# Performance work log

Measured on AMD Instinct MI355X. Metric: run time of the kernel, lower is better.

## Reference

```python
import jax, jax.numpy as jnp
import numpy as np
import math

B, T, E, H, HS = 8, 2048, 384, 6, 64

def setup_inputs() -> dict:
    key = jax.random.key(0)
    ks = jax.random.split(key, 5)
    scale = 1.0 / math.sqrt(E)
    return {
        "x": jax.random.normal(ks[0], (B, T, E), dtype=jnp.float32),
        "Wq": jax.random.normal(ks[1], (H, E, HS), dtype=jnp.float32) * scale,
        "Wk": jax.random.normal(ks[2], (H, E, HS), dtype=jnp.float32) * scale,
        "Wv": jax.random.normal(ks[3], (H, E, HS), dtype=jnp.float32) * scale,
        "Wo": jax.random.normal(ks[4], (H, HS, E), dtype=jnp.float32) * (1.0 / math.sqrt(HS)),
    }

def reference(x, Wq, Wk, Wv, Wo):
    # x: [B,T,E]; per-head projections batched over heads.
    q = jnp.einsum('bte,hed->bhtd', x, Wq)  # [B,H,T,HS]
    k = jnp.einsum('bte,hed->bhtd', x, Wk)
    v = jnp.einsum('bte,hed->bhtd', x, Wv)
    scores = jnp.einsum('bhid,bhjd->bhij', q, k)  # [B,H,T,T]
    # Faithful to source: MULTIPLICATIVE tril mask (masked logits become 0, not -inf),
    # then scale by 1/sqrt(head_size), then softmax.
    t = x.shape[1]
    tril = jnp.tril(jnp.ones((t, t), dtype=scores.dtype))
    scores = scores * tril / math.sqrt(HS)
    attn = jax.nn.softmax(scores, axis=-1)
    ctx = jnp.einsum('bhij,bhjd->bhid', attn, v)  # [B,H,T,HS]
    # Per-head output projection to embed dim, summed over heads (source accumulates).
    out = jnp.einsum('bhtd,hde->bte', ctx, Wo)  # [B,T,E]
    return out
```

## Files before the change

### kernel.cpp

```cpp
#include <hip/hip_runtime.h>
#include <math.h>

#define BBATCH 8
#define TSEQ   2048
#define EDIM   384
#define NHEAD  6
#define DHEAD  64
#define NBH    48
#define QTILE  128
#define NQT    16
#define NW1    442368
#define NW2    147456
#define XSZ    6291456
#define KVSZ   6291456

typedef __attribute__((ext_vector_type(8)))  short bf16x8;
typedef __attribute__((ext_vector_type(16))) float f32x16;
typedef __attribute__((ext_vector_type(2)))  int   i32x2;
typedef unsigned short u16;
typedef unsigned int   u32;

#define MFMA(a, b, c) __builtin_amdgcn_mfma_f32_32x32x16_bf16(a, b, c, 0, 0, 0)

__device__ __forceinline__ u16 f2bf(float f) {
  u32 u = __float_as_uint(f);
  return (u16)((u + 0x7fffu + ((u >> 16) & 1u)) >> 16);
}
__device__ __forceinline__ float bf2f(u16 h) {
  return __uint_as_float(((u32)h) << 16);
}
__device__ __forceinline__ bf16x8 mk8(u32 w0, u32 w1, u32 w2, u32 w3) {
  union { u32 u[4]; bf16x8 v; } t;
  t.u[0] = w0; t.u[1] = w1; t.u[2] = w2; t.u[3] = w3;
  return t.v;
}

__global__ __launch_bounds__(256) void prep_w_k(
    const float* __restrict__ Wq, const float* __restrict__ Wk,
    const float* __restrict__ Wv, const float* __restrict__ Wo,
    u16* __restrict__ wtH, u16* __restrict__ wtL,
    u16* __restrict__ woH, u16* __restrict__ woL) {
  int idx = blockIdx.x * 256 + threadIdx.x;
  if (idx < NW1) {
    int d = idx & 63;
    int q = idx >> 6;
    int e = q % EDIM;
    int ph = q / EDIM;
    const float* W = (ph < 6) ? Wq : (ph < 12) ? Wk : Wv;
    int h = ph % 6;
    float v = W[((size_t)h * EDIM + e) * DHEAD + d];
    u16 hi = f2bf(v);
    size_t o = ((size_t)ph * DHEAD + d) * EDIM + e;
    wtH[o] = hi;
    wtL[o] = f2bf(v - bf2f(hi));
  } else {
    int o = idx - NW1;
    int eo = o % EDIM;
    int hd = o / EDIM;
    float v = Wo[(size_t)hd * EDIM + eo];
    u16 hi = f2bf(v);
    size_t oo = (size_t)eo * EDIM + hd;
    woH[oo] = hi;
    woL[oo] = f2bf(v - bf2f(hi));
  }
}

__global__ __launch_bounds__(256) void splitx_k(
    const float* __restrict__ x, u16* __restrict__ xh, u16* __restrict__ xl) {
  int i = (blockIdx.x * 256 + threadIdx.x) * 8;
  float4 a = *(const float4*)(x + i);
  float4 b = *(const float4*)(x + i + 4);
  u16 h0 = f2bf(a.x), h1 = f2bf(a.y), h2 = f2bf(a.z), h3 = f2bf(a.w);
  u16 h4 = f2bf(b.x), h5 = f2bf(b.y), h6 = f2bf(b.z), h7 = f2bf(b.w);
  uint4 H, L;
  H.x = (u32)h0 | ((u32)h1 << 16); H.y = (u32)h2 | ((u32)h3 << 16);
  H.z = (u32)h4 | ((u32)h5 << 16); H.w = (u32)h6 | ((u32)h7 << 16);
  L.x = (u32)f2bf(a.x - bf2f(h0)) | ((u32)f2bf(a.y - bf2f(h1)) << 16);
  L.y = (u32)f2bf(a.z - bf2f(h2)) | ((u32)f2bf(a.w - bf2f(h3)) << 16);
  L.z = (u32)f2bf(b.x - bf2f(h4)) | ((u32)f2bf(b.y - bf2f(h5)) << 16);
  L.w = (u32)f2bf(b.z - bf2f(h6)) | ((u32)f2bf(b.w - bf2f(h7)) << 16);
  *(uint4*)(xh + i) = H;
  *(uint4*)(xl + i) = L;
}

__global__ __launch_bounds__(256, 2) void proj_k(
    const u16* __restrict__ xh, const u16* __restrict__ xl,
    const u16* __restrict__ wtH, const u16* __restrict__ wtL,
    u16* __restrict__ qh, u16* __restrict__ ql,
    u16* __restrict__ kh, u16* __restrict__ kl,
    u16* __restrict__ vTh, u16* __restrict__ vTl,
    float* __restrict__ psum) {
  __shared__ __align__(16) unsigned char sm[32768];
  const int tid = threadIdx.x;
  const int w = tid >> 6, l = tid & 63, lh = l >> 5, l31 = l & 31;
  const int gid = ((blockIdx.x & 7) * 288) + ((int)blockIdx.x >> 3);
  const int bx = gid / 18, ph = gid % 18;
  const int p = ph / 6, h = ph % 6;
  const int bt0 = bx * 128;
  const u16* __restrict__ wBh = wtH + (size_t)ph * DHEAD * EDIM;
  const u16* __restrict__ wBl = wtL + (size_t)ph * DHEAD * EDIM;

  f32x16 acc0, acc1;
#pragma unroll
  for (int i = 0; i < 16; ++i) { acc0[i] = 0.f; acc1[i] = 0.f; }

  for (int k0 = 0; k0 < EDIM; k0 += 64) {
    __syncthreads();
#pragma unroll
    for (int i = 0; i < 4; ++i) {
      int c = tid + i * 256;
      int r = c >> 3, s = c & 7;
      int off = (r * 128 + s * 16) ^ ((r & 7) << 4);
      size_t g = (size_t)(bt0 + r) * EDIM + k0 + s * 8;
      *(uint4*)(sm + off) = *(const uint4*)(xh + g);
      *(uint4*)(sm + 16384 + off) = *(const uint4*)(xl + g);
    }
    __syncthreads();
    const int arow = 32 * w + l31;
#pragma unroll
    for (int ks = 0; ks < 4; ++ks) {
      int aoff = (arow * 128 + ks * 32 + 16 * lh) ^ ((arow & 7) << 4);
      bf16x8 aH = *(const bf16x8*)(sm + aoff);
      bf16x8 aL = *(const bf16x8*)(sm + 16384 + aoff);
      int eoff = k0 + ks * 16 + 8 * lh;
      size_t b0 = (size_t)l31 * EDIM + eoff;
      size_t b1 = (size_t)(32 + l31) * EDIM + eoff;
      bf16x8 bH0 = *(const bf16x8*)(wBh + b0);
      bf16x8 bL0 = *(const bf16x8*)(wBl + b0);
      bf16x8 bH1 = *(const bf16x8*)(wBh + b1);
      bf16x8 bL1 = *(const bf16x8*)(wBl + b1);
      acc0 = MFMA(aH, bH0, acc0); acc0 = MFMA(aH, bL0, acc0); acc0 = MFMA(aL, bH0, acc0);
      acc1 = MFMA(aH, bH1, acc1); acc1 = MFMA(aH, bL1, acc1); acc1 = MFMA(aL, bH1, acc1);
    }
  }

  const int b = bt0 >> 11, t0b = bt0 & (TSEQ - 1);
  const int bh = b * NHEAD + h;
  const float scale = (p == 0) ? 0.125f : 1.0f;

  if (p < 2) {
    u16* oH = (p == 0) ? qh : kh;
    u16* oL = (p == 0) ? ql : kl;
#pragma unroll
    for (int reg = 0; reg < 16; ++reg) {
      int row = (reg & 3) + 8 * (reg >> 2) + 4 * lh + 32 * w;
      size_t base = ((size_t)bh * TSEQ + t0b + row) * DHEAD;
      float v0 = acc0[reg] * scale, v1 = acc1[reg] * scale;
      u16 h0 = f2bf(v0), h1 = f2bf(v1);
      oH[base + l31] = h0;       oL[base + l31] = f2bf(v0 - bf2f(h0));
      oH[base + 32 + l31] = h1;  oL[base + 32 + l31] = f2bf(v1 - bf2f(h1));
    }
  } else {
    u16* T = (u16*)sm;
#pragma unroll
    for (int half = 0; half < 2; ++half) {
      __syncthreads();
#pragma unroll
      for (int reg = 0; reg < 16; ++reg) {
        int t = (reg & 3) + 8 * (reg >> 2) + 4 * lh + 32 * w;
        float v0 = acc0[reg], v1 = acc1[reg];
        u16 e0, e1;
        if (half == 0) { e0 = f2bf(v0); e1 = f2bf(v1); }
        else {
          u16 a0 = f2bf(v0), a1 = f2bf(v1);
          e0 = f2bf(v0 - bf2f(a0)); e1 = f2bf(v1 - bf2f(a1));
        }
        T[l31 * 132 + t] = e0;
        T[(32 + l31) * 132 + t] = e1;
      }
      __syncthreads();
      u16* dst = half ? vTl : vTh;
#pragma unroll
      for (int i = 0; i < 8; ++i) {
        int c = tid + i * 256;
        int d = c >> 5, s = c & 31;
        uint2 val = *(const uint2*)(T + d * 132 + s * 4);
        *(uint2*)(dst + ((size_t)bh * DHEAD + d) * TSEQ + t0b + s * 4) = val;
      }
    }
    float s0 = 0.f, s1 = 0.f;
#pragma unroll
    for (int reg = 0; reg < 16; ++reg) { s0 += acc0[reg]; s1 += acc1[reg]; }
    s0 += __shfl_xor(s0, 32);
    s1 += __shfl_xor(s1, 32);
    __syncthreads();
    float* ps = (float*)sm;
    if (lh == 0) { ps[w * 64 + l31] = s0; ps[w * 64 + 32 + l31] = s1; }
    __syncthreads();
    if (tid < 64) {
      float t = ps[tid] + ps[64 + tid] + ps[128 + tid] + ps[192 + tid];
      int tile = t0b >> 7;
      psum[((size_t)bh * NQT + tile) * DHEAD + tid] = t;
    }
  }
}

__global__ __launch_bounds__(64, 3) void attn_k(
    const u16* __restrict__ qh, const u16* __restrict__ ql,
    const u16* __restrict__ kh, const u16* __restrict__ kl,
    const u16* __restrict__ vTh, const u16* __restrict__ vTl,
    const float* __restrict__ psum,
    u16* __restrict__ cxh, u16* __restrict__ cxl) {
  const int l = threadIdx.x;
  const int lh = l >> 5, l31 = l & 31;
  const int xcd = blockIdx.x & 7;
  const int idx = (int)blockIdx.x >> 3;
  const int qt = (NQT - 1) - (idx / 24);
  const int rem = idx % 24;
  const int bhl = rem >> 2, ws = rem & 3;
  const int bh = xcd * 6 + bhl;
  const int b = bh / NHEAD, h = bh % NHEAD;
  const int t0 = qt * QTILE;
  const size_t kvb = (size_t)bh * TSEQ * DHEAD;

  const int qglo = t0 + 32 * ws;
  bf16x8 qfH[4], qfL[4];
#pragma unroll
  for (int ks = 0; ks < 4; ++ks) {
    size_t g = kvb + (size_t)(qglo + l31) * DHEAD + ks * 16 + 8 * lh;
    qfH[ks] = *(const bf16x8*)(qh + g);
    qfL[ks] = *(const bf16x8*)(ql + g);
  }

  f32x16 accO0, accO1;
#pragma unroll
  for (int i = 0; i < 16; ++i) { accO0[i] = 0.f; accO1[i] = 0.f; }
  float lrun = 0.f;
  const int qg = qglo + l31;
  const int S = 2 * (qt + 1);

  for (int jt = 0; jt < S; ++jt) {
#pragma unroll
    for (int jh = 0; jh < 2; ++jh) {
      f32x16 accSa, accSb;
#pragma unroll
      for (int i = 0; i < 16; ++i) { accSa[i] = 0.f; accSb[i] = 0.f; }
      const size_t krow = kvb + (size_t)(jt * 64 + jh * 32 + l31) * DHEAD;
      __builtin_amdgcn_s_setprio(1);
#pragma unroll
      for (int ks = 0; ks < 4; ++ks) {
        size_t g = krow + ks * 16 + 8 * lh;
        bf16x8 aH = *(const bf16x8*)(kh + g);
        bf16x8 aL = *(const bf16x8*)(kl + g);
        accSa = MFMA(aH, qfH[ks], accSa);
        accSb = MFMA(aH, qfL[ks], accSb);
        accSb = MFMA(aL, qfH[ks], accSb);
      }
      __builtin_amdgcn_s_setprio(0);
      f32x16 accS;
#pragma unroll
      for (int i = 0; i < 16; ++i) accS[i] = accSa[i] + accSb[i];

      const int jb = jt * 64 + jh * 32 + 4 * lh;
      float ps = 0.f;
#pragma unroll
      for (int ml = 0; ml < 2; ++ml) {
        int rb = ml * 8;
        u32 hw[4], lw[4];
#pragma unroll
        for (int pr = 0; pr < 4; ++pr) {
          int r0 = rb + 2 * pr;
          int jg0 = jb + (r0 & 3) + 8 * (r0 >> 2);
          float s0 = (jg0 > qg) ? 0.f : accS[r0];
          float s1 = ((jg0 + 1) > qg) ? 0.f : accS[r0 + 1];
          float p0 = __expf(s0), p1 = __expf(s1);
          ps += p0 + p1;
          u16 a0 = f2bf(p0), a1 = f2bf(p1);
          hw[pr] = (u32)a0 | ((u32)a1 << 16);
          lw[pr] = (u32)f2bf(p0 - bf2f(a0)) | ((u32)f2bf(p1 - bf2f(a1)) << 16);
        }
        i32x2 s1 = __builtin_amdgcn_permlane32_swap((int)hw[0], (int)hw[2], false, false);
        i32x2 s2 = __builtin_amdgcn_permlane32_swap((int)hw[1], (int)hw[3], false, false);
        bf16x8 pH = mk8((u32)s1.x, (u32)s2.x, (u32)s1.y, (u32)s2.y);
        i32x2 t1 = __builtin_amdgcn_permlane32_swap((int)lw[0], (int)lw[2], false, false);
        i32x2 t2 = __builtin_amdgcn_permlane32_swap((int)lw[1], (int)lw[3], false, false);
        bf16x8 pL = mk8((u32)t1.x, (u32)t2.x, (u32)t1.y, (u32)t2.y);
        int m = jh * 2 + ml;
        size_t vcol = (size_t)jt * 64 + m * 16 + 8 * lh;
        size_t v0 = kvb + (size_t)l31 * TSEQ + vcol;
        size_t v1 = kvb + (size_t)(32 + l31) * TSEQ + vcol;
        bf16x8 vH0 = *(const bf16x8*)(vTh + v0);
        bf16x8 vL0 = *(const bf16x8*)(vTl + v0);
        bf16x8 vH1 = *(const bf16x8*)(vTh + v1);
        bf16x8 vL1 = *(const bf16x8*)(vTl + v1);
        __builtin_amdgcn_s_setprio(1);
        accO0 = MFMA(pH, vH0, accO0); accO0 = MFMA(pH, vL0, accO0); accO0 = MFMA(pL, vH0, accO0);
        accO1 = MFMA(pH, vH1, accO1); accO1 = MFMA(pH, vL1, accO1); accO1 = MFMA(pL, vH1, accO1);
        __builtin_amdgcn_s_setprio(0);
      }
      lrun += ps;
    }
  }

  lrun += __shfl_xor(lrun, 32);
  lrun += (float)(TSEQ - S * 64);
  {
    float tl0 = 0.f, tl1 = 0.f;
    for (int tt = qt + 1; tt < NQT; ++tt) {
      const float* ps = psum + ((size_t)bh * NQT + tt) * DHEAD;
      tl0 += ps[l31];
      tl1 += ps[32 + l31];
    }
#pragma unroll
    for (int reg = 0; reg < 16; ++reg) { accO0[reg] += tl0; accO1[reg] += tl1; }
  }
#pragma unroll
  for (int reg = 0; reg < 16; ++reg) {
    int qrow = (reg & 3) + 8 * (reg >> 2) + 4 * lh;
    float lq = __shfl(lrun, qrow);
    float inv = 1.f / lq;
    int t = qglo + qrow;
    size_t o = ((size_t)b * TSEQ + t) * EDIM + h * DHEAD;
    float v0 = accO0[reg] * inv, v1 = accO1[reg] * inv;
    u16 h0 = f2bf(v0), h1 = f2bf(v1);
    cxh[o + l31] = h0;       cxl[o + l31] = f2bf(v0 - bf2f(h0));
    cxh[o + 32 + l31] = h1;  cxl[o + 32 + l31] = f2bf(v1 - bf2f(h1));
  }
}

__global__ __launch_bounds__(256, 2) void outproj_k(
    const u16* __restrict__ cxh, const u16* __restrict__ cxl,
    const u16* __restrict__ woH, const u16* __restrict__ woL,
    float* __restrict__ out) {
  __shared__ __align__(16) unsigned char sm[32768];
  const int tid = threadIdx.x;
  const int w = tid >> 6, l = tid & 63, lh = l >> 5, l31 = l & 31;
  const int gid = ((blockIdx.x & 7) * 96) + ((int)blockIdx.x >> 3);
  const int bx = gid / 6, ey = gid % 6;
  const int bt0 = bx * 128, e0 = ey * 64;

  f32x16 acc0, acc1;
#pragma unroll
  for (int i = 0; i < 16; ++i) { acc0[i] = 0.f; acc1[i] = 0.f; }

  for (int k0 = 0; k0 < EDIM; k0 += 64) {
    __syncthreads();
#pragma unroll
    for (int i = 0; i < 4; ++i) {
      int c = tid + i * 256;
      int r = c >> 3, s = c & 7;
      int off = (r * 128 + s * 16) ^ ((r & 7) << 4);
      size_t g = (size_t)(bt0 + r) * EDIM + k0 + s * 8;
      *(uint4*)(sm + off) = *(const uint4*)(cxh + g);
      *(uint4*)(sm + 16384 + off) = *(const uint4*)(cxl + g);
    }
    __syncthreads();
    const int arow = 32 * w + l31;
#pragma unroll
    for (int ks = 0; ks < 4; ++ks) {
      int aoff = (arow * 128 + ks * 32 + 16 * lh) ^ ((arow & 7) << 4);
      bf16x8 aH = *(const bf16x8*)(sm + aoff);
      bf16x8 aL = *(const bf16x8*)(sm + 16384 + aoff);
      int hdoff = k0 + ks * 16 + 8 * lh;
      size_t b0 = (size_t)(e0 + l31) * EDIM + hdoff;
      size_t b1 = (size_t)(e0 + 32 + l31) * EDIM + hdoff;
      bf16x8 bH0 = *(const bf16x8*)(woH + b0);
      bf16x8 bL0 = *(const bf16x8*)(woL + b0);
      bf16x8 bH1 = *(const bf16x8*)(woH + b1);
      bf16x8 bL1 = *(const bf16x8*)(woL + b1);
      acc0 = MFMA(aH, bH0, acc0); acc0 = MFMA(aH, bL0, acc0); acc0 = MFMA(aL, bH0, acc0);
      acc1 = MFMA(aH, bH1, acc1); acc1 = MFMA(aH, bL1, acc1); acc1 = MFMA(aL, bH1, acc1);
    }
  }
#pragma unroll
  for (int reg = 0; reg < 16; ++reg) {
    int row = (reg & 3) + 8 * (reg >> 2) + 4 * lh + 32 * w;
    size_t o = (size_t)(bt0 + row) * EDIM + e0;
    out[o + l31] = acc0[reg];
    out[o + 32 + l31] = acc1[reg];
  }
}

extern "C" void kernel_launch(void* const* d_in, const int* in_sizes, int n_in,
                              void* d_out, int out_size, void* d_ws, size_t ws_size,
                              hipStream_t stream) {
  (void)in_sizes; (void)n_in; (void)out_size; (void)ws_size;
  const float* x  = (const float*)d_in[0];
  const float* Wq = (const float*)d_in[1];
  const float* Wk = (const float*)d_in[2];
  const float* Wv = (const float*)d_in[3];
  const float* Wo = (const float*)d_in[4];
  float* out = (float*)d_out;

  u16* qh  = (u16*)d_ws;
  u16* ql  = qh + KVSZ;
  u16* kh  = ql + KVSZ;
  u16* kl  = kh + KVSZ;
  u16* vTh = kl + KVSZ;
  u16* vTl = vTh + KVSZ;
  u16* xh  = vTl + KVSZ;
  u16* xl  = xh + XSZ;
  u16* wtH = xl + XSZ;
  u16* wtL = wtH + NW1;
  u16* woH = wtL + NW1;
  u16* woL = woH + NW2;
  float* psum = (float*)(woL + NW2);
  u16* cxh = xh;
  u16* cxl = xl;

  hipLaunchKernelGGL(prep_w_k, dim3((NW1 + NW2) / 256), dim3(256), 0, stream,
                     Wq, Wk, Wv, Wo, wtH, wtL, woH, woL);
  hipLaunchKernelGGL(splitx_k, dim3(XSZ / 2048), dim3(256), 0, stream, x, xh, xl);
  hipLaunchKernelGGL(proj_k, dim3(2304), dim3(256), 0, stream,
                     xh, xl, wtH, wtL, qh, ql, kh, kl, vTh, vTl, psum);
  hipLaunchKernelGGL(attn_k, dim3(3072), dim3(64), 0, stream,
                     qh, ql, kh, kl, vTh, vTl, psum, cxh, cxl);
  hipLaunchKernelGGL(outproj_k, dim3(768), dim3(256), 0, stream,
                     cxh, cxl, woH, woL, out);
}
```

Measured before the change: 460.6 us.

## Software-pipeline K loads in attention and use packed bf16 conversion

The attention inner loop is rewritten as 32-key steps that prefetch the next step's K fragments into a double-buffered register set (KA/KB) while the current step's MFMAs run, and it loads V earlier within each step. The manual bf16 rounding is replaced by the packed __float22bfloat162_rn intrinsic. Launch bounds are changed: attn_k drops its occupancy hint from 3 to 2 to leave room for the extra registers, and proj_k and outproj_k raise theirs from 2 to 4. The register prefetch is meant to hide global load latency, but it costs more VGPRs and fewer resident waves in attention.

New measurement: 452.8 us. No clear change (-1.7%).

```diff
diff --git a/kernel.cpp b/kernel.cpp
--- a/kernel.cpp
+++ b/kernel.cpp
@@ -1,4 +1,5 @@
 #include <hip/hip_runtime.h>
+#include <hip/hip_bf16.h>
 #include <math.h>
 
 #define BBATCH 8
@@ -28,6 +29,10 @@
 }
 __device__ __forceinline__ float bf2f(u16 h) {
   return __uint_as_float(((u32)h) << 16);
+}
+__device__ __forceinline__ u32 pk2(float a, float b) {
+  __hip_bfloat162 t = __float22bfloat162_rn(make_float2(a, b));
+  union { __hip_bfloat162 v; u32 u; } c; c.v = t; return c.u;
 }
 __device__ __forceinline__ bf16x8 mk8(u32 w0, u32 w1, u32 w2, u32 w3) {
   union { u32 u[4]; bf16x8 v; } t;
@@ -83,7 +88,7 @@
   *(uint4*)(xl + i) = L;
 }
 
-__global__ __launch_bounds__(256, 2) void proj_k(
+__global__ __launch_bounds__(256, 4) void proj_k(
     const u16* __restrict__ xh, const u16* __restrict__ xl,
     const u16* __restrict__ wtH, const u16* __restrict__ wtL,
     u16* __restrict__ qh, u16* __restrict__ ql,
@@ -195,7 +200,86 @@
   }
 }
 
-__global__ __launch_bounds__(64, 3) void attn_k(
+#define LOADK(DST, S_) do {                                                  \
+    size_t ldk_g = kvb + (size_t)((S_) * 32 + l31) * DHEAD + 8 * lh;         \
+    DST[0] = *(const bf16x8*)(kh + ldk_g);                                   \
+    DST[1] = *(const bf16x8*)(kh + ldk_g + 16);                              \
+    DST[2] = *(const bf16x8*)(kh + ldk_g + 32);                              \
+    DST[3] = *(const bf16x8*)(kh + ldk_g + 48);                              \
+    DST[4] = *(const bf16x8*)(kl + ldk_g);                                   \
+    DST[5] = *(const bf16x8*)(kl + ldk_g + 16);                              \
+    DST[6] = *(const bf16x8*)(kl + ldk_g + 32);                              \
+    DST[7] = *(const bf16x8*)(kl + ldk_g + 48);                              \
+  } while (0)
+
+#define STEP(CUR, NXT, S_) do {                                              \
+    const int st_ = (S_);                                                    \
+    LOADK(NXT, (st_ + 1 < smax2) ? st_ + 1 : smax2 - 1);                     \
+    f32x16 aSa, aSb;                                                         \
+    _Pragma("unroll")                                                        \
+    for (int i_ = 0; i_ < 16; ++i_) { aSa[i_] = 0.f; aSb[i_] = 0.f; }        \
+    __builtin_amdgcn_s_setprio(1);                                           \
+    aSa = MFMA(CUR[0], qfH[0], aSa); aSb = MFMA(CUR[0], qfL[0], aSb);        \
+    aSb = MFMA(CUR[4], qfH[0], aSb);                                         \
+    aSa = MFMA(CUR[1], qfH[1], aSa); aSb = MFMA(CUR[1], qfL[1], aSb);        \
+    aSb = MFMA(CUR[5], qfH[1], aSb);                                         \
+    aSa = MFMA(CUR[2], qfH[2], aSa); aSb = MFMA(CUR[2], qfL[2], aSb);        \
+    aSb = MFMA(CUR[6], qfH[2], aSb);                                         \
+    aSa = MFMA(CUR[3], qfH[3], aSa); aSb = MFMA(CUR[3], qfL[3], aSb);        \
+    aSb = MFMA(CUR[7], qfH[3], aSb);                                         \
+    __builtin_amdgcn_s_setprio(0);                                           \
+    size_t vr0_ = kvb + (size_t)l31 * TSEQ + (size_t)st_ * 32 + 8 * lh;      \
+    size_t vr1_ = vr0_ + (size_t)32 * TSEQ;                                  \
+    bf16x8 v0H0 = *(const bf16x8*)(vTh + vr0_);                              \
+    bf16x8 v0L0 = *(const bf16x8*)(vTl + vr0_);                              \
+    bf16x8 v1H0 = *(const bf16x8*)(vTh + vr1_);                              \
+    bf16x8 v1L0 = *(const bf16x8*)(vTl + vr1_);                              \
+    bf16x8 v0H1 = *(const bf16x8*)(vTh + vr0_ + 16);                         \
+    bf16x8 v0L1 = *(const bf16x8*)(vTl + vr0_ + 16);                         \
+    bf16x8 v1H1 = *(const bf16x8*)(vTh + vr1_ + 16);                         \
+    bf16x8 v1L1 = *(const bf16x8*)(vTl + vr1_ + 16);                         \
+    f32x16 accS_;                                                            \
+    _Pragma("unroll")                                                        \
+    for (int i_ = 0; i_ < 16; ++i_) accS_[i_] = aSa[i_] + aSb[i_];           \
+    const int jb_ = st_ * 32 + 4 * lh;                                       \
+    float ps_ = 0.f;                                                         \
+    _Pragma("unroll")                                                        \
+    for (int ml_ = 0; ml_ < 2; ++ml_) {                                      \
+      u32 hw_[4], lw_[4];                                                    \
+      _Pragma("unroll")                                                      \
+      for (int pr_ = 0; pr_ < 4; ++pr_) {                                    \
+        int r0_ = ml_ * 8 + 2 * pr_;                                         \
+        int jg_ = jb_ + (r0_ & 3) + 8 * (r0_ >> 2);                          \
+        float s0_ = (jg_ > qg) ? 0.f : accS_[r0_];                           \
+        float s1_ = (jg_ + 1 > qg) ? 0.f : accS_[r0_ + 1];                   \
+        float p0_ = __expf(s0_), p1_ = __expf(s1_);                          \
+        ps_ += p0_ + p1_;                                                    \
+        u32 w_ = pk2(p0_, p1_);                                              \
+        hw_[pr_] = w_;                                                       \
+        lw_[pr_] = pk2(p0_ - __uint_as_float(w_ << 16),                      \
+                       p1_ - __uint_as_float(w_ & 0xffff0000u));             \
+      }                                                                      \
+      i32x2 sA_ = __builtin_amdgcn_permlane32_swap((int)hw_[0], (int)hw_[2], false, false); \
+      i32x2 sB_ = __builtin_amdgcn_permlane32_swap((int)hw_[1], (int)hw_[3], false, false); \
+      bf16x8 pH_ = mk8((u32)sA_.x, (u32)sB_.x, (u32)sA_.y, (u32)sB_.y);      \
+      i32x2 tA_ = __builtin_amdgcn_permlane32_swap((int)lw_[0], (int)lw_[2], false, false); \
+      i32x2 tB_ = __builtin_amdgcn_permlane32_swap((int)lw_[1], (int)lw_[3], false, false); \
+      bf16x8 pL_ = mk8((u32)tA_.x, (u32)tB_.x, (u32)tA_.y, (u32)tB_.y);      \
+      bf16x8 vh0_ = ml_ ? v0H1 : v0H0;                                       \
+      bf16x8 vl0_ = ml_ ? v0L1 : v0L0;                                       \
+      bf16x8 vh1_ = ml_ ? v1H1 : v1H0;                                       \
+      bf16x8 vl1_ = ml_ ? v1L1 : v1L0;                                       \
+      __builtin_amdgcn_s_setprio(1);                                         \
+      accO0 = MFMA(pH_, vh0_, accO0); accO0 = MFMA(pH_, vl0_, accO0);        \
+      accO0 = MFMA(pL_, vh0_, accO0);                                        \
+      accO1 = MFMA(pH_, vh1_, accO1); accO1 = MFMA(pH_, vl1_, accO1);        \
+      accO1 = MFMA(pL_, vh1_, accO1);                                        \
+      __builtin_amdgcn_s_setprio(0);                                         \
+    }                                                                        \
+    lrun += ps_;                                                             \
+  } while (0)
+
+__global__ __launch_bounds__(64, 2) void attn_k(
     const u16* __restrict__ qh, const u16* __restrict__ ql,
     const u16* __restrict__ kh, const u16* __restrict__ kl,
     const u16* __restrict__ vTh, const u16* __restrict__ vTl,
@@ -210,10 +294,9 @@
   const int bhl = rem >> 2, ws = rem & 3;
   const int bh = xcd * 6 + bhl;
   const int b = bh / NHEAD, h = bh % NHEAD;
-  const int t0 = qt * QTILE;
   const size_t kvb = (size_t)bh * TSEQ * DHEAD;
 
-  const int qglo = t0 + 32 * ws;
+  const int qglo = qt * QTILE + 32 * ws;
   bf16x8 qfH[4], qfL[4];
 #pragma unroll
   for (int ks = 0; ks < 4; ++ks) {
@@ -227,73 +310,18 @@
   for (int i = 0; i < 16; ++i) { accO0[i] = 0.f; accO1[i] = 0.f; }
   float lrun = 0.f;
   const int qg = qglo + l31;
-  const int S = 2 * (qt + 1);
-
-  for (int jt = 0; jt < S; ++jt) {
-#pragma unroll
-    for (int jh = 0; jh < 2; ++jh) {
-      f32x16 accSa, accSb;
-#pragma unroll
-      for (int i = 0; i < 16; ++i) { accSa[i] = 0.f; accSb[i] = 0.f; }
-      const size_t krow = kvb + (size_t)(jt * 64 + jh * 32 + l31) * DHEAD;
-      __builtin_amdgcn_s_setprio(1);
-#pragma unroll
-      for (int ks = 0; ks < 4; ++ks) {
-        size_t g = krow + ks * 16 + 8 * lh;
-        bf16x8 aH = *(const bf16x8*)(kh + g);
-        bf16x8 aL = *(const bf16x8*)(kl + g);
-        accSa = MFMA(aH, qfH[ks], accSa);
-        accSb = MFMA(aH, qfL[ks], accSb);
-        accSb = MFMA(aL, qfH[ks], accSb);
-      }
-      __builtin_amdgcn_s_setprio(0);
-      f32x16 accS;
-#pragma unroll
-      for (int i = 0; i < 16; ++i) accS[i] = accSa[i] + accSb[i];
-
-      const int jb = jt * 64 + jh * 32 + 4 * lh;
-      float ps = 0.f;
-#pragma unroll
-      for (int ml = 0; ml < 2; ++ml) {
-        int rb = ml * 8;
-        u32 hw[4], lw[4];
-#pragma unroll
-        for (int pr = 0; pr < 4; ++pr) {
-          int r0 = rb + 2 * pr;
-          int jg0 = jb + (r0 & 3) + 8 * (r0 >> 2);
-          float s0 = (jg0 > qg) ? 0.f : accS[r0];
-          float s1 = ((jg0 + 1) > qg) ? 0.f : accS[r0 + 1];
-          float p0 = __expf(s0), p1 = __expf(s1);
-          ps += p0 + p1;
-          u16 a0 = f2bf(p0), a1 = f2bf(p1);
-          hw[pr] = (u32)a0 | ((u32)a1 << 16);
-          lw[pr] = (u32)f2bf(p0 - bf2f(a0)) | ((u32)f2bf(p1 - bf2f(a1)) << 16);
-        }
-        i32x2 s1 = __builtin_amdgcn_permlane32_swap((int)hw[0], (int)hw[2], false, false);
-        i32x2 s2 = __builtin_amdgcn_permlane32_swap((int)hw[1], (int)hw[3], false, false);
-        bf16x8 pH = mk8((u32)s1.x, (u32)s2.x, (u32)s1.y, (u32)s2.y);
-        i32x2 t1 = __builtin_amdgcn_permlane32_swap((int)lw[0], (int)lw[2], false, false);
-        i32x2 t2 = __builtin_amdgcn_permlane32_swap((int)lw[1], (int)lw[3], false, false);
-        bf16x8 pL = mk8((u32)t1.x, (u32)t2.x, (u32)t1.y, (u32)t2.y);
-        int m = jh * 2 + ml;
-        size_t vcol = (size_t)jt * 64 + m * 16 + 8 * lh;
-        size_t v0 = kvb + (size_t)l31 * TSEQ + vcol;
-        size_t v1 = kvb + (size_t)(32 + l31) * TSEQ + vcol;
-        bf16x8 vH0 = *(const bf16x8*)(vTh + v0);
-        bf16x8 vL0 = *(const bf16x8*)(vTl + v0);
-        bf16x8 vH1 = *(const bf16x8*)(vTh + v1);
-        bf16x8 vL1 = *(const bf16x8*)(vTl + v1);
-        __builtin_amdgcn_s_setprio(1);
-        accO0 = MFMA(pH, vH0, accO0); accO0 = MFMA(pH, vL0, accO0); accO0 = MFMA(pL, vH0, accO0);
-        accO1 = MFMA(pH, vH1, accO1); accO1 = MFMA(pH, vL1, accO1); accO1 = MFMA(pL, vH1, accO1);
-        __builtin_amdgcn_s_setprio(0);
-      }
-      lrun += ps;
-    }
+  const int smax2 = 4 * (qt + 1);
+
+  bf16x8 KA[8], KB[8];
+  LOADK(KA, 0);
+
+  for (int s = 0; s < smax2; s += 2) {
+    STEP(KA, KB, s);
+    STEP(KB, KA, s + 1);
   }
 
   lrun += __shfl_xor(lrun, 32);
-  lrun += (float)(TSEQ - S * 64);
+  lrun += (float)(TSEQ - smax2 * 32);
   {
     float tl0 = 0.f, tl1 = 0.f;
     for (int tt = qt + 1; tt < NQT; ++tt) {
@@ -317,8 +345,10 @@
     cxh[o + 32 + l31] = h1;  cxl[o + 32 + l31] = f2bf(v1 - bf2f(h1));
   }
 }
-
-__global__ __launch_bounds__(256, 2) void outproj_k(
+#undef STEP
+#undef LOADK
+
+__global__ __launch_bounds__(256, 4) void outproj_k(
     const u16* __restrict__ cxh, const u16* __restrict__ cxl,
     const u16* __restrict__ woH, const u16* __restrict__ woL,
     float* __restrict__ out) {
```
